# Kernel optimization log

Hardware: AMD Instinct MI355X
Metric: run time of the kernel (lower is better)

## Reference

```python
import jax, jax.numpy as jnp
import numpy as np

B, LP, LQ, H = 32, 2048, 512, 1024

def setup_inputs() -> dict:
    key = jax.random.key(0)
    k1, k2, k3, k4 = jax.random.split(key, 4)
    p_encode = jax.random.normal(k1, (B, LP, H), dtype=jnp.float32)
    q_encode = jax.random.normal(k2, (B, LQ, H), dtype=jnp.float32)
    # nn.Linear(H, H): weight [out, in], bias [out]
    bound = 1.0 / np.sqrt(H)
    G_weight = jax.random.uniform(k3, (H, H), dtype=jnp.float32, minval=-bound, maxval=bound)
    G_bias = jax.random.uniform(k4, (H,), dtype=jnp.float32, minval=-bound, maxval=bound)
    return {"p_encode": p_encode, "q_encode": q_encode, "G_weight": G_weight, "G_bias": G_bias}

def reference(p_encode, q_encode, G_weight, G_bias):
    # q_project = transpose(G(q_encode), -2, -1): [B, H, LQ]
    q_proj = jnp.einsum('bqh,oh->bqo', q_encode, G_weight) + G_bias  # [B, LQ, H]
    # att_matrix = bmm(p_encode, q_project^T): [B, LP, LQ]
    att = jnp.einsum('bph,bqh->bpq', p_encode, q_proj)
    # m_p = softmax over LQ (dim=-1) @ q_encode -> [B, LP, H]
    m_p = jnp.einsum('bpq,bqh->bph', jax.nn.softmax(att, axis=-1), q_encode)
    # m_q = softmax over LP (dim=-2), transposed, @ p_encode -> [B, LQ, H]
    m_q = jnp.einsum('bpq,bph->bqh', jax.nn.softmax(att, axis=-2), p_encode)
    return (m_p, m_q)
```

## Files before the change

kernel.cpp:

```cpp
#include <hip/hip_runtime.h>

typedef _Float16 half_t;
typedef _Float16 f16x8 __attribute__((ext_vector_type(8)));
typedef _Float16 f16x4 __attribute__((ext_vector_type(4)));
typedef float    f32x4 __attribute__((ext_vector_type(4)));
typedef float    f32x16 __attribute__((ext_vector_type(16)));

typedef const __attribute__((address_space(1))) void cg_void;
typedef __attribute__((address_space(3))) void lds_void;

#define BB 32
#define LP 2048
#define LQ 512
#define HH 1024

enum { M_QPROJ = 0, M_OUT32 = 1 };

__global__ void cvt16_k(const float* __restrict__ w, half_t* __restrict__ o) {
  long i = ((long)blockIdx.x * 256 + threadIdx.x) * 4;
  f32x4 v = *(const f32x4*)(w + i);
  f16x4 h;
  h[0] = (half_t)v[0]; h[1] = (half_t)v[1]; h[2] = (half_t)v[2]; h[3] = (half_t)v[3];
  *(f16x4*)(o + i) = h;
}

__global__ __launch_bounds__(256) void cvt2_k(const float* __restrict__ qe,
                                              half_t* __restrict__ q16o,
                                              half_t* __restrict__ qT16o,
                                              const float* __restrict__ pe,
                                              half_t* __restrict__ p16o,
                                              half_t* __restrict__ pT16o) {
  __shared__ half_t tile[64 * 64];
  const int byg = blockIdx.y;
  const float* in; half_t* rm; half_t* tr; int R, r0;
  if (byg < 8) { in = qe; rm = q16o; tr = qT16o; R = LQ; r0 = byg * 64; }
  else         { in = pe; rm = p16o; tr = pT16o; R = LP; r0 = (byg - 8) * 64; }
  const int C = HH;
  const long zb = blockIdx.z;
  const float* src = in + zb * (long)R * C;
  half_t* dstT = tr + zb * (long)C * R;
  half_t* dstR = rm + zb * (long)R * C;
  const int c0 = blockIdx.x * 64;
  const int t = threadIdx.x;
  const int cl = (t & 15) * 4;
  const int rl = t >> 4;
#pragma unroll
  for (int rr = 0; rr < 4; rr++) {
    int r = rr * 16 + rl;
    f32x4 v = *(const f32x4*)(src + (long)(r0 + r) * C + c0 + cl);
    f16x4 h;
#pragma unroll
    for (int j = 0; j < 4; j++) {
      h[j] = (half_t)v[j];
      int c = cl + j;
      tile[c * 64 + (r ^ (((c >> 3) & 7) << 3))] = h[j];
    }
    *(f16x4*)(dstR + (long)(r0 + r) * C + c0 + cl) = h;
  }
  __syncthreads();
  const int c = t >> 2;
  const int rch = (t & 3) * 16;
  const int m = (c >> 3) & 7;
  const int B0 = c * 64 + (rch ^ ((m << 3) & 48));
  const int hi = (m & 1) << 3;
  f16x8 g0 = *(const f16x8*)&tile[B0 + hi];
  f16x8 g1 = *(const f16x8*)&tile[B0 + (8 ^ hi)];
  half_t* dp = dstT + (long)(c0 + c) * R + r0 + rch;
  *(f16x8*)dp = g0;
  *(f16x8*)(dp + 8) = g1;
}

__global__ __launch_bounds__(256) void cfin_k(const float* __restrict__ pmg,
                                              const float* __restrict__ psg,
                                              float* __restrict__ cmax,
                                              float* __restrict__ cinv) {
  long i = (long)blockIdx.x * 256 + threadIdx.x;
  long b = i / LQ, q = i - b * LQ;
  const float* mp = pmg + (b * 16) * LQ + q;
  const float* sp = psg + (b * 16) * LQ + q;
  float m = -3e38f, s = 0.f;
#pragma unroll
  for (int t = 0; t < 16; t++) {
    float mm = mp[(long)t * LQ], ss = sp[(long)t * LQ];
    float nm = fmaxf(m, mm);
    s = s * __expf(m - nm) + ss * __expf(mm - nm);
    m = nm;
  }
  cmax[i] = m;
  cinv[i] = 1.f / s;
}

__global__ __launch_bounds__(256) void pq_k(const half_t* __restrict__ E,
                                            half_t* __restrict__ out,
                                            const float* __restrict__ pmg,
                                            const float* __restrict__ cmax,
                                            const float* __restrict__ cinv) {
  __shared__ half_t tile[64 * 64];
  const long zb = blockIdx.z;
  const half_t* src = E + zb * (long)LP * LQ;
  half_t* dst = out + zb * (long)LQ * LP;
  const int r0 = blockIdx.y * 64, c0 = blockIdx.x * 64;
  const int tIdx = r0 >> 7;
  const int t = threadIdx.x;
  const int cl = (t & 15) * 4;
  const int rl = t >> 4;
  f32x4 tm = *(const f32x4*)(pmg + ((long)zb * 16 + tIdx) * LQ + c0 + cl);
  f32x4 cm = *(const f32x4*)(cmax + (long)zb * LQ + c0 + cl);
  f32x4 ci = *(const f32x4*)(cinv + (long)zb * LQ + c0 + cl);
  float sc[4];
#pragma unroll
  for (int j = 0; j < 4; j++) sc[j] = __expf(tm[j] - cm[j]) * ci[j];
#pragma unroll
  for (int rr = 0; rr < 4; rr++) {
    int r = rr * 16 + rl;
    f16x4 v = *(const f16x4*)(src + (long)(r0 + r) * LQ + c0 + cl);
#pragma unroll
    for (int j = 0; j < 4; j++) {
      float x = (float)v[j] * sc[j];
      int c = cl + j;
      tile[c * 64 + (r ^ (((c >> 3) & 7) << 3))] = (half_t)x;
    }
  }
  __syncthreads();
  const int c = t >> 2;
  const int rch = (t & 3) * 16;
  const int m = (c >> 3) & 7;
  const int B0 = c * 64 + (rch ^ ((m << 3) & 48));
  const int hi = (m & 1) << 3;
  f16x8 g0 = *(const f16x8*)&tile[B0 + hi];
  f16x8 g1 = *(const f16x8*)&tile[B0 + (8 ^ hi)];
  half_t* dp = dst + (long)(c0 + c) * LP + r0 + rch;
  *(f16x8*)dp = g0;
  *(f16x8*)(dp + 8) = g1;
}

template<int ROWS>
__device__ __forceinline__ void stage_op(const half_t* src, int ld,
                                         half_t* lds_base, int wid, int lane) {
  const int goff = (((lane & 3) ^ ((lane >> 3) & 3)) << 3);
#pragma unroll
  for (int j = 0; j < ROWS / 128; ++j) {
    int row = j * 128 + wid * 16 + (lane >> 2);
    const half_t* g = src + (long)row * ld + goff;
    __builtin_amdgcn_global_load_lds((cg_void*)g,
        (lds_void*)(lds_base + j * 4096 + wid * 512), 16, 0, 0);
  }
}

__device__ __forceinline__ void stage4(const half_t* src, int ld,
                                       half_t* lds_base, int wid, int lane) {
  const int goff = (((lane & 3) ^ ((lane >> 3) & 3)) << 3);
#pragma unroll
  for (int j = 0; j < 2; ++j) {
    int row = j * 64 + wid * 16 + (lane >> 2);
    const half_t* g = src + (long)row * ld + goff;
    __builtin_amdgcn_global_load_lds((cg_void*)g,
        (lds_void*)(lds_base + j * 2048 + wid * 512), 16, 0, 0);
  }
}

__device__ __forceinline__ void xcd_swz(long lid, long nwg, long& out) {
  const long q8 = nwg >> 3, r8 = nwg & 7;
  const long xcd = lid & 7, rest = lid >> 3;
  out = (xcd < r8 ? xcd * (q8 + 1) : r8 * (q8 + 1) + (xcd - r8) * q8) + rest;
}

__global__ __launch_bounds__(512, 2) void attf_k(
    const half_t* __restrict__ Ap, const half_t* __restrict__ Bp,
    half_t* __restrict__ PpO, half_t* __restrict__ EO,
    float* __restrict__ pmg, float* __restrict__ psg) {
  __shared__ __align__(16) half_t As[3 * 4096];
  __shared__ __align__(16) half_t Bs[3 * 16384];
  __shared__ float rmL[4][128];
  __shared__ float cmL[2][512];
  __shared__ float rsL[4][128];
  __shared__ float csL[2][512];

  const int nby = gridDim.y;
  long lid;
  xcd_swz(blockIdx.y + (long)nby * blockIdx.z, (long)nby * gridDim.z, lid);
  const int by = (int)(lid % nby);
  const int bz = (int)(lid / nby);

  const int t0 = threadIdx.x;
  const int lane = t0 & 63;
  const int wid = t0 >> 6;
  const int wm = wid >> 2, wn = wid & 3;
  const int m0 = by * 128;

  const half_t* Abase = Ap + ((long)bz * LP + m0) * HH;
  const half_t* Bbase = Bp + (long)bz * LQ * HH;

  const int c5 = lane & 31, hi = lane >> 5;
  const int sx = (c5 >> 1) & 3;
  const int ofs0 = c5 * 32 + ((hi ^ sx) << 3);
  const int ofs1 = c5 * 32 + (((2 | hi) ^ sx) << 3);

  f32x16 acc[2][4] = {};
  const int NT = HH / 32;

#pragma unroll
  for (int tt = 0; tt < 2; ++tt) {
    stage_op<128>(Abase + tt * 32, HH, As + tt * 4096, wid, lane);
    stage_op<512>(Bbase + tt * 32, HH, Bs + tt * 16384, wid, lane);
  }

  for (int t = 0; t < NT; ++t) {
    if (t + 1 < NT) asm volatile("s_waitcnt vmcnt(5)" ::: "memory");
    else            asm volatile("s_waitcnt vmcnt(0)" ::: "memory");
    __builtin_amdgcn_s_barrier();
    asm volatile("" ::: "memory");

    const half_t* Au = As + (t % 3) * 4096;
    const half_t* Bu = Bs + (t % 3) * 16384;
    f16x8 af[2][2], bf[4][2];
#pragma unroll
    for (int mf = 0; mf < 2; ++mf) {
      const half_t* p = Au + (wm * 64 + mf * 32) * 32;
      af[mf][0] = *(const f16x8*)(p + ofs0);
      af[mf][1] = *(const f16x8*)(p + ofs1);
    }
#pragma unroll
    for (int nf = 0; nf < 4; ++nf) {
      const half_t* p = Bu + (wn * 128 + nf * 32) * 32;
      bf[nf][0] = *(const f16x8*)(p + ofs0);
      bf[nf][1] = *(const f16x8*)(p + ofs1);
    }
    if (t + 2 < NT) {
      const int u2 = (t + 2) % 3;
      stage_op<128>(Abase + (t + 2) * 32, HH, As + u2 * 4096, wid, lane);
      stage_op<512>(Bbase + (t + 2) * 32, HH, Bs + u2 * 16384, wid, lane);
    }
    __builtin_amdgcn_s_setprio(1);
#pragma unroll
    for (int mf = 0; mf < 2; ++mf)
#pragma unroll
      for (int nf = 0; nf < 4; ++nf) {
        acc[mf][nf] = __builtin_amdgcn_mfma_f32_32x32x16_f16(af[mf][0], bf[nf][0], acc[mf][nf], 0, 0, 0);
        acc[mf][nf] = __builtin_amdgcn_mfma_f32_32x32x16_f16(af[mf][1], bf[nf][1], acc[mf][nf], 0, 0, 0);
      }
    __builtin_amdgcn_s_setprio(0);
  }

  float rmv[2][16], cmv[4];
#pragma unroll
  for (int m = 0; m < 2; ++m)
#pragma unroll
    for (int r = 0; r < 16; ++r) {
      float v = fmaxf(fmaxf(acc[m][0][r], acc[m][1][r]), fmaxf(acc[m][2][r], acc[m][3][r]));
#pragma unroll
      for (int o = 1; o < 32; o <<= 1) v = fmaxf(v, __shfl_xor(v, o, 64));
      rmv[m][r] = v;
    }
#pragma unroll
  for (int n = 0; n < 4; ++n) {
    float v = acc[0][n][0];
#pragma unroll
    for (int m = 0; m < 2; ++m)
#pragma unroll
      for (int r = 0; r < 16; ++r) v = fmaxf(v, acc[m][n][r]);
    v = fmaxf(v, __shfl_xor(v, 32, 64));
    cmv[n] = v;
  }
  if (c5 < 16) {
#pragma unroll
    for (int m = 0; m < 2; ++m)
      rmL[wn][wm * 64 + m * 32 + (c5 & 3) + 8 * (c5 >> 2) + 4 * hi] = rmv[m][c5];
  }
  if (hi == 0) {
#pragma unroll
    for (int n = 0; n < 4; ++n) cmL[wm][wn * 128 + n * 32 + c5] = cmv[n];
  }
  __syncthreads();
  if (t0 < 128)
    rmL[0][t0] = fmaxf(fmaxf(rmL[0][t0], rmL[1][t0]), fmaxf(rmL[2][t0], rmL[3][t0]));
  {
    float cm2 = fmaxf(cmL[0][t0 & 511], cmL[1][t0 & 511]);
    cmL[0][t0 & 511] = cm2;
    pmg[((long)bz * 16 + by) * LQ + (t0 & 511)] = cm2;
  }
  __syncthreads();
#pragma unroll
  for (int m = 0; m < 2; ++m)
#pragma unroll
    for (int r = 0; r < 16; ++r)
      rmv[m][r] = rmL[0][wm * 64 + m * 32 + (r & 3) + 8 * (r >> 2) + 4 * hi];
#pragma unroll
  for (int n = 0; n < 4; ++n) cmv[n] = cmL[0][wn * 128 + n * 32 + c5];

  half_t* EB = EO + (long)bz * LP * LQ;
  float csW[4] = {0.f, 0.f, 0.f, 0.f};
  float rowS[2][16];
#pragma unroll
  for (int m = 0; m < 2; ++m)
#pragma unroll
    for (int r = 0; r < 16; ++r) {
      long grow = (long)(m0 + wm * 64 + m * 32 + (r & 3) + 8 * (r >> 2) + 4 * hi) * LQ;
      float s = 0.f;
#pragma unroll
      for (int n = 0; n < 4; ++n) {
        float a = acc[m][n][r];
        float e = __expf(a - cmv[n]);
        float p = __expf(a - rmv[m][r]);
        csW[n] += e;
        EB[grow + wn * 128 + n * 32 + c5] = (half_t)e;
        acc[m][n][r] = p;
        s += p;
      }
#pragma unroll
      for (int o = 1; o < 32; o <<= 1) s += __shfl_xor(s, o, 64);
      rowS[m][r] = s;
    }
#pragma unroll
  for (int n = 0; n < 4; ++n) csW[n] += __shfl_xor(csW[n], 32, 64);
  if (c5 < 16) {
#pragma unroll
    for (int m = 0; m < 2; ++m)
      rsL[wn][wm * 64 + m * 32 + (c5 & 3) + 8 * (c5 >> 2) + 4 * hi] = rowS[m][c5];
  }
  if (hi == 0) {
#pragma unroll
    for (int n = 0; n < 4; ++n) csL[wm][wn * 128 + n * 32 + c5] = csW[n];
  }
  __syncthreads();
  if (t0 < 128)
    rsL[0][t0] = 1.f / (rsL[0][t0] + rsL[1][t0] + rsL[2][t0] + rsL[3][t0]);
  psg[((long)bz * 16 + by) * LQ + (t0 & 511)] = csL[0][t0 & 511] + csL[1][t0 & 511];
  __syncthreads();

  half_t* PpB = PpO + (long)bz * LP * LQ;
#pragma unroll
  for (int m = 0; m < 2; ++m)
#pragma unroll
    for (int r = 0; r < 16; ++r) {
      int row = wm * 64 + m * 32 + (r & 3) + 8 * (r >> 2) + 4 * hi;
      long grow = (long)(m0 + row) * LQ;
      float ri = rsL[0][row];
#pragma unroll
      for (int n = 0; n < 4; ++n)
        PpB[grow + wn * 128 + n * 32 + c5] = (half_t)(acc[m][n][r] * ri);
    }
}

template<int MODE>
__device__ __forceinline__ void core97(const half_t* __restrict__ Ab,
                                       const half_t* __restrict__ Bb,
                                       void* __restrict__ cB,
                                       const float* __restrict__ biasB,
                                       int lda, int ldb, int ldc, int K) {
  __shared__ __align__(16) half_t As[2][4096];
  __shared__ __align__(16) half_t Bs[2][4096];

  const int t0 = threadIdx.x;
  const int lane = t0 & 63;
  const int wid = t0 >> 6;
  const int wm = wid >> 1, wn = wid & 1;
  const int fr = lane & 15, fs = lane >> 4;
  const int fbase = fr * 32 + ((fs ^ ((fr >> 1) & 3)) << 3);

  f32x4 acc[4][4] = {};
  const int NT = K >> 5;

  stage4(Ab, lda, As[0], wid, lane);
  stage4(Bb, ldb, Bs[0], wid, lane);
  __syncthreads();

  int cur = 0;
  for (int t = 0; t < NT; ++t) {
    if (t + 1 < NT) {
      stage4(Ab + (t + 1) * 32, lda, As[cur ^ 1], wid, lane);
      stage4(Bb + (t + 1) * 32, ldb, Bs[cur ^ 1], wid, lane);
    }
    f16x8 af[4], bf[4];
#pragma unroll
    for (int f = 0; f < 4; ++f) af[f] = *(const f16x8*)&As[cur][(wm * 64 + f * 16) * 32 + fbase];
#pragma unroll
    for (int f = 0; f < 4; ++f) bf[f] = *(const f16x8*)&Bs[cur][(wn * 64 + f * 16) * 32 + fbase];
    __builtin_amdgcn_s_setprio(1);
#pragma unroll
    for (int fm = 0; fm < 4; ++fm)
#pragma unroll
      for (int fn = 0; fn < 4; ++fn)
        acc[fm][fn] = __builtin_amdgcn_mfma_f32_16x16x32_f16(af[fm], bf[fn], acc[fm][fn], 0, 0, 0);
    __builtin_amdgcn_s_setprio(0);
    __syncthreads();
    cur ^= 1;
  }

  const int r0 = (lane >> 4) * 4;
#pragma unroll
  for (int fn = 0; fn < 4; ++fn) {
    int col = wn * 64 + fn * 16 + fr;
    float bv = 0.f;
    if constexpr (MODE == M_QPROJ) bv = biasB[col];
#pragma unroll
    for (int fm = 0; fm < 4; ++fm) {
      int row = wm * 64 + fm * 16 + r0;
#pragma unroll
      for (int j = 0; j < 4; j++) {
        if constexpr (MODE == M_QPROJ)
          ((half_t*)cB)[(long)(row + j) * ldc + col] = (half_t)(acc[fm][fn][j] + bv);
        else
          ((float*)cB)[(long)(row + j) * ldc + col] = acc[fm][fn][j];
      }
    }
  }
}

__global__ __launch_bounds__(256, 3) void gemmq_k(const half_t* __restrict__ q16,
                                                  const half_t* __restrict__ w16,
                                                  half_t* __restrict__ qpj,
                                                  const float* __restrict__ Gb) {
  const int nbx = gridDim.x, nby = gridDim.y;
  long lid;
  xcd_swz(blockIdx.x + (long)nbx * blockIdx.y, (long)nbx * nby, lid);
  const int bx = (int)(lid % nbx);
  const int by = (int)(lid / nbx);
  core97<M_QPROJ>(q16 + (long)(by * 128) * HH,
                  w16 + (long)(bx * 128) * HH,
                  qpj + (long)(by * 128) * HH + bx * 128,
                  Gb + bx * 128, HH, HH, HH, HH);
}

__global__ __launch_bounds__(256, 3) void gemm2_k(
    const half_t* __restrict__ Pp, const half_t* __restrict__ qT16, float* __restrict__ m_p,
    const half_t* __restrict__ Pq, const half_t* __restrict__ pT16, float* __restrict__ m_q) {
  long lid;
  xcd_swz(blockIdx.x + 8L * (blockIdx.y + 20L * blockIdx.z), 8L * 20 * 32, lid);
  const int bx = (int)(lid % 8);
  const long tmp = lid / 8;
  const int by = (int)(tmp % 20);
  const int bz = (int)(tmp / 20);

  if (by < 16) {
    core97<M_OUT32>(Pp + (long)bz * LP * LQ + (long)(by * 128) * LQ,
                    qT16 + (long)bz * HH * LQ + (long)(bx * 128) * LQ,
                    m_p + (long)bz * LP * HH + (long)(by * 128) * HH + bx * 128,
                    nullptr, LQ, LQ, HH, LQ);
  } else {
    const int qy = by - 16;
    core97<M_OUT32>(Pq + (long)bz * LQ * LP + (long)(qy * 128) * LP,
                    pT16 + (long)bz * HH * LP + (long)(bx * 128) * LP,
                    m_q + (long)bz * LQ * HH + (long)(qy * 128) * HH + bx * 128,
                    nullptr, LP, LP, HH, LP);
  }
}

extern "C" void kernel_launch(void* const* d_in, const int* in_sizes, int n_in,
                              void* d_out, int out_size, void* d_ws, size_t ws_size,
                              hipStream_t stream) {
  const float* p_enc = (const float*)d_in[0];
  const float* q_enc = (const float*)d_in[1];
  const float* Gw    = (const float*)d_in[2];
  const float* Gb    = (const float*)d_in[3];
  float* m_p = (float*)d_out;
  float* m_q = m_p + (long)BB * LP * HH;

  half_t* w16   = (half_t*)d_ws;
  half_t* q16   = w16 + (long)HH * HH;
  half_t* qT16  = q16 + (long)BB * LQ * HH;
  half_t* qpj16 = qT16 + (long)BB * HH * LQ;
  half_t* p16   = qpj16 + (long)BB * LQ * HH;
  half_t* pT16  = p16 + (long)BB * LP * HH;
  half_t* Pp    = pT16 + (long)BB * HH * LP;
  half_t* Ebuf  = Pp + (long)BB * LP * LQ;
  half_t* Pq    = Ebuf + (long)BB * LP * LQ;
  float*  cmaxb = (float*)(Pq + (long)BB * LQ * LP);
  float*  cinvb = cmaxb + (long)BB * LQ;
  float*  pmg   = cinvb + (long)BB * LQ;
  float*  psg   = pmg + (long)BB * 16 * LQ;

  cvt16_k<<<HH * HH / 1024, 256, 0, stream>>>(Gw, w16);

  cvt2_k<<<dim3(HH / 64, 40, BB), 256, 0, stream>>>(q_enc, q16, qT16, p_enc, p16, pT16);

  gemmq_k<<<dim3(HH / 128, BB * LQ / 128, 1), 256, 0, stream>>>(q16, w16, qpj16, Gb);

  attf_k<<<dim3(1, LP / 128, BB), 512, 0, stream>>>(p16, qpj16, Pp, Ebuf, pmg, psg);

  cfin_k<<<BB * LQ / 256, 256, 0, stream>>>(pmg, psg, cmaxb, cinvb);
  pq_k<<<dim3(LQ / 64, LP / 64, BB), 256, 0, stream>>>(Ebuf, Pq, pmg, cmaxb, cinvb);

  gemm2_k<<<dim3(8, 20, BB), 256, 0, stream>>>(Pp, qT16, m_p, Pq, pT16, m_q);
}
```

Before: 552.3 us.

## Use 256x256 tiles with triple-buffered LDS pipeline in projection and output GEMMs

Replaces the 128x128, 256-thread, double-buffered GEMM core with a 256x256, 512-thread core that uses three LDS stages, a prefetch depth of two, and split A/B staging interleaved with two MFMA halves per k-step. Larger tiles raise arithmetic intensity and cut redundant global loads. The deeper pipeline with explicit vmcnt waits aims to hide load latency. gemm2 now schedules the long-K m_q tiles first to reduce tail imbalance. The trade-off is heavier register and LDS use (96KB of LDS), lower occupancy, and fewer blocks for the projection GEMM.

```diff
diff --git a/kernel.cpp b/kernel.cpp
--- a/kernel.cpp
+++ b/kernel.cpp
@@ -147,18 +147,6 @@
   }
 }
 
-__device__ __forceinline__ void stage4(const half_t* src, int ld,
-                                       half_t* lds_base, int wid, int lane) {
-  const int goff = (((lane & 3) ^ ((lane >> 3) & 3)) << 3);
-#pragma unroll
-  for (int j = 0; j < 2; ++j) {
-    int row = j * 64 + wid * 16 + (lane >> 2);
-    const half_t* g = src + (long)row * ld + goff;
-    __builtin_amdgcn_global_load_lds((cg_void*)g,
-        (lds_void*)(lds_base + j * 2048 + wid * 512), 16, 0, 0);
-  }
-}
-
 __device__ __forceinline__ void xcd_swz(long lid, long nwg, long& out) {
   const long q8 = nwg >> 3, r8 = nwg & 7;
   const long xcd = lid & 7, rest = lid >> 3;
@@ -343,106 +331,126 @@
 }
 
 template<int MODE>
-__device__ __forceinline__ void core97(const half_t* __restrict__ Ab,
-                                       const half_t* __restrict__ Bb,
-                                       void* __restrict__ cB,
-                                       const float* __restrict__ biasB,
-                                       int lda, int ldb, int ldc, int K) {
-  __shared__ __align__(16) half_t As[2][4096];
-  __shared__ __align__(16) half_t Bs[2][4096];
+__device__ __forceinline__ void core8(const half_t* __restrict__ Ab,
+                                      const half_t* __restrict__ Bb,
+                                      void* __restrict__ cB,
+                                      const float* __restrict__ biasB,
+                                      int lda, int ldb, int ldc, int K) {
+  __shared__ __align__(16) half_t As[3][8192];
+  __shared__ __align__(16) half_t Bs[3][8192];
 
   const int t0 = threadIdx.x;
   const int lane = t0 & 63;
   const int wid = t0 >> 6;
-  const int wm = wid >> 1, wn = wid & 1;
+  const int wm = wid >> 2, wn = wid & 3;
   const int fr = lane & 15, fs = lane >> 4;
   const int fbase = fr * 32 + ((fs ^ ((fr >> 1) & 3)) << 3);
 
-  f32x4 acc[4][4] = {};
+  f32x4 acc[8][4] = {};
   const int NT = K >> 5;
 
-  stage4(Ab, lda, As[0], wid, lane);
-  stage4(Bb, ldb, Bs[0], wid, lane);
-  __syncthreads();
-
-  int cur = 0;
+  stage_op<256>(Ab, lda, As[0], wid, lane);
+  stage_op<256>(Bb, ldb, Bs[0], wid, lane);
+  stage_op<256>(Ab + 32, lda, As[1], wid, lane);
+  stage_op<256>(Bb + 32, ldb, Bs[1], wid, lane);
+  asm volatile("s_waitcnt vmcnt(4)" ::: "memory");
+  __builtin_amdgcn_s_barrier();
+  asm volatile("" ::: "memory");
+
   for (int t = 0; t < NT; ++t) {
-    if (t + 1 < NT) {
-      stage4(Ab + (t + 1) * 32, lda, As[cur ^ 1], wid, lane);
-      stage4(Bb + (t + 1) * 32, ldb, Bs[cur ^ 1], wid, lane);
-    }
-    f16x8 af[4], bf[4];
-#pragma unroll
-    for (int f = 0; f < 4; ++f) af[f] = *(const f16x8*)&As[cur][(wm * 64 + f * 16) * 32 + fbase];
-#pragma unroll
-    for (int f = 0; f < 4; ++f) bf[f] = *(const f16x8*)&Bs[cur][(wn * 64 + f * 16) * 32 + fbase];
+    const half_t* Au = As[t % 3];
+    const half_t* Bu = Bs[t % 3];
+    f16x8 af[4], bf[4], ag[4];
+#pragma unroll
+    for (int mf = 0; mf < 4; ++mf)
+      af[mf] = *(const f16x8*)&Au[(wm * 128 + mf * 16) * 32 + fbase];
+#pragma unroll
+    for (int nf = 0; nf < 4; ++nf)
+      bf[nf] = *(const f16x8*)&Bu[(wn * 64 + nf * 16) * 32 + fbase];
+    if (t + 2 < NT) stage_op<256>(Ab + (t + 2) * 32, lda, As[(t + 2) % 3], wid, lane);
+    __builtin_amdgcn_s_barrier();
+    asm volatile("" ::: "memory");
     __builtin_amdgcn_s_setprio(1);
 #pragma unroll
-    for (int fm = 0; fm < 4; ++fm)
-#pragma unroll
-      for (int fn = 0; fn < 4; ++fn)
-        acc[fm][fn] = __builtin_amdgcn_mfma_f32_16x16x32_f16(af[fm], bf[fn], acc[fm][fn], 0, 0, 0);
+    for (int mf = 0; mf < 4; ++mf)
+#pragma unroll
+      for (int nf = 0; nf < 4; ++nf)
+        acc[mf][nf] = __builtin_amdgcn_mfma_f32_16x16x32_f16(af[mf], bf[nf], acc[mf][nf], 0, 0, 0);
     __builtin_amdgcn_s_setprio(0);
-    __syncthreads();
-    cur ^= 1;
+    __builtin_amdgcn_s_barrier();
+    asm volatile("" ::: "memory");
+#pragma unroll
+    for (int mf = 0; mf < 4; ++mf)
+      ag[mf] = *(const f16x8*)&Au[(wm * 128 + 64 + mf * 16) * 32 + fbase];
+    if (t + 2 < NT) stage_op<256>(Bb + (t + 2) * 32, ldb, Bs[(t + 2) % 3], wid, lane);
+    __builtin_amdgcn_s_setprio(1);
+#pragma unroll
+    for (int mf = 0; mf < 4; ++mf)
+#pragma unroll
+      for (int nf = 0; nf < 4; ++nf)
+        acc[4 + mf][nf] = __builtin_amdgcn_mfma_f32_16x16x32_f16(ag[mf], bf[nf], acc[4 + mf][nf], 0, 0, 0);
+    __builtin_amdgcn_s_setprio(0);
+    if (t + 2 < NT)      asm volatile("s_waitcnt vmcnt(4)" ::: "memory");
+    else if (t + 1 < NT) asm volatile("s_waitcnt vmcnt(0)" ::: "memory");
+    __builtin_amdgcn_s_barrier();
+    asm volatile("" ::: "memory");
   }
 
   const int r0 = (lane >> 4) * 4;
 #pragma unroll
-  for (int fn = 0; fn < 4; ++fn) {
-    int col = wn * 64 + fn * 16 + fr;
+  for (int nf = 0; nf < 4; ++nf) {
+    int col = wn * 64 + nf * 16 + fr;
     float bv = 0.f;
     if constexpr (MODE == M_QPROJ) bv = biasB[col];
 #pragma unroll
-    for (int fm = 0; fm < 4; ++fm) {
-      int row = wm * 64 + fm * 16 + r0;
+    for (int i = 0; i < 8; ++i) {
+      int row = wm * 128 + (i >> 2) * 64 + (i & 3) * 16 + r0;
 #pragma unroll
       for (int j = 0; j < 4; j++) {
         if constexpr (MODE == M_QPROJ)
-          ((half_t*)cB)[(long)(row + j) * ldc + col] = (half_t)(acc[fm][fn][j] + bv);
+          ((half_t*)cB)[(long)(row + j) * ldc + col] = (half_t)(acc[i][nf][j] + bv);
         else
-          ((float*)cB)[(long)(row + j) * ldc + col] = acc[fm][fn][j];
+          ((float*)cB)[(long)(row + j) * ldc + col] = acc[i][nf][j];
       }
     }
   }
 }
 
-__global__ __launch_bounds__(256, 3) void gemmq_k(const half_t* __restrict__ q16,
+__global__ __launch_bounds__(512, 2) void gemmq_k(const half_t* __restrict__ q16,
                                                   const half_t* __restrict__ w16,
                                                   half_t* __restrict__ qpj,
                                                   const float* __restrict__ Gb) {
-  const int nbx = gridDim.x, nby = gridDim.y;
   long lid;
-  xcd_swz(blockIdx.x + (long)nbx * blockIdx.y, (long)nbx * nby, lid);
-  const int bx = (int)(lid % nbx);
-  const int by = (int)(lid / nbx);
-  core97<M_QPROJ>(q16 + (long)(by * 128) * HH,
-                  w16 + (long)(bx * 128) * HH,
-                  qpj + (long)(by * 128) * HH + bx * 128,
-                  Gb + bx * 128, HH, HH, HH, HH);
-}
-
-__global__ __launch_bounds__(256, 3) void gemm2_k(
+  xcd_swz(blockIdx.x + 4L * blockIdx.y, 4L * gridDim.y, lid);
+  const int bx = (int)(lid % 4);
+  const int by = (int)(lid / 4);
+  core8<M_QPROJ>(q16 + (long)(by * 256) * HH,
+                 w16 + (long)(bx * 256) * HH,
+                 qpj + (long)(by * 256) * HH + bx * 256,
+                 Gb + bx * 256, HH, HH, HH, HH);
+}
+
+__global__ __launch_bounds__(512, 2) void gemm2_k(
     const half_t* __restrict__ Pp, const half_t* __restrict__ qT16, float* __restrict__ m_p,
     const half_t* __restrict__ Pq, const half_t* __restrict__ pT16, float* __restrict__ m_q) {
   long lid;
-  xcd_swz(blockIdx.x + 8L * (blockIdx.y + 20L * blockIdx.z), 8L * 20 * 32, lid);
-  const int bx = (int)(lid % 8);
-  const long tmp = lid / 8;
-  const int by = (int)(tmp % 20);
-  const int bz = (int)(tmp / 20);
-
-  if (by < 16) {
-    core97<M_OUT32>(Pp + (long)bz * LP * LQ + (long)(by * 128) * LQ,
-                    qT16 + (long)bz * HH * LQ + (long)(bx * 128) * LQ,
-                    m_p + (long)bz * LP * HH + (long)(by * 128) * HH + bx * 128,
-                    nullptr, LQ, LQ, HH, LQ);
+  xcd_swz(blockIdx.x + 4L * (blockIdx.y + 10L * blockIdx.z), 4L * 10 * 32, lid);
+  const int bx = (int)(lid % 4);
+  const long tmp = lid / 4;
+  const int by = (int)(tmp % 10);
+  const int bz = (int)(tmp / 10);
+
+  if (by < 2) {
+    core8<M_OUT32>(Pq + (long)bz * LQ * LP + (long)(by * 256) * LP,
+                   pT16 + (long)bz * HH * LP + (long)(bx * 256) * LP,
+                   m_q + (long)bz * LQ * HH + (long)(by * 256) * HH + bx * 256,
+                   nullptr, LP, LP, HH, LP);
   } else {
-    const int qy = by - 16;
-    core97<M_OUT32>(Pq + (long)bz * LQ * LP + (long)(qy * 128) * LP,
-                    pT16 + (long)bz * HH * LP + (long)(bx * 128) * LP,
-                    m_q + (long)bz * LQ * HH + (long)(qy * 128) * HH + bx * 128,
-                    nullptr, LP, LP, HH, LP);
+    const int py = by - 2;
+    core8<M_OUT32>(Pp + (long)bz * LP * LQ + (long)(py * 256) * LQ,
+                   qT16 + (long)bz * HH * LQ + (long)(bx * 256) * LQ,
+                   m_p + (long)bz * LP * HH + (long)(py * 256) * HH + bx * 256,
+                   nullptr, LQ, LQ, HH, LQ);
   }
 }
 
@@ -474,12 +482,12 @@
 
   cvt2_k<<<dim3(HH / 64, 40, BB), 256, 0, stream>>>(q_enc, q16, qT16, p_enc, p16, pT16);
 
-  gemmq_k<<<dim3(HH / 128, BB * LQ / 128, 1), 256, 0, stream>>>(q16, w16, qpj16, Gb);
+  gemmq_k<<<dim3(4, 64, 1), 512, 0, stream>>>(q16, w16, qpj16, Gb);
 
   attf_k<<<dim3(1, LP / 128, BB), 512, 0, stream>>>(p16, qpj16, Pp, Ebuf, pmg, psg);
 
   cfin_k<<<BB * LQ / 256, 256, 0, stream>>>(pmg, psg, cmaxb, cinvb);
   pq_k<<<dim3(LQ / 64, LP / 64, BB), 256, 0, stream>>>(Ebuf, Pq, pmg, cmaxb, cinvb);
 
-  gemm2_k<<<dim3(8, 20, BB), 256, 0, stream>>>(Pp, qT16, m_p, Pq, pT16, m_q);
-}
+  gemm2_k<<<dim3(4, 10, BB), 512, 0, stream>>>(Pp, qT16, m_p, Pq, pT16, m_q);
+}
```

Result: slower. 564.9 us (+2.3%).
